# Performance work log

Hardware: AMD Instinct MI355X
Metric: run time of the kernel (lower is better)

Reference implementation:

```python
import jax, jax.numpy as jnp
import numpy as np

B, H, N, C, E, D, L_OUT, LAYERS = 16, 64, 512, 3, 128, 32, 12, 2


def setup_inputs() -> dict:
    key = jax.random.key(0)
    ks = jax.random.split(key, 16)
    nrm = lambda k, s, sc=1.0: jax.random.normal(k, s, jnp.float32) * sc
    adj = jax.random.uniform(ks[0], (N, N), jnp.float32)
    adj = adj / adj.sum(axis=-1, keepdims=True)  # row-normalized prior adjacency
    return {
        "x_input": nrm(ks[1], (B, H, N, C)),
        "adj": adj,
        "Wf": nrm(ks[2], (3, E, 3 * C), 0.1),
        "Uf": nrm(ks[3], (3, E, E), 0.05),
        "bf": jnp.zeros((3, E), jnp.float32),
        "E1f": nrm(ks[4], (N, D)),
        "E2f": nrm(ks[5], (N, D)),
        "Wb": nrm(ks[6], (3, E, 3 * C), 0.1),
        "Ub": nrm(ks[7], (3, E, E), 0.05),
        "bb": jnp.zeros((3, E), jnp.float32),
        "E1b": nrm(ks[8], (N, D)),
        "E2b": nrm(ks[9], (N, D)),
        "dec_w": nrm(ks[10], (L_OUT, LAYERS, 2 * E), 0.05),  # Conv2d(layer_num->out_len, k=(1,2E)) squeezed
        "dec_b": jnp.zeros((L_OUT,), jnp.float32),
        "out_w": nrm(ks[11], (L_OUT, L_OUT), 0.1),  # 1x1 Conv2d squeezed
        "out_b": jnp.zeros((L_OUT,), jnp.float32),
    }


def _cell_step(c, xt, adj, A_dyn, W, U, b):
    # Graph-coupled GRU cell (IBNCell): xt [B,C,N], c [B,E,N].
    msg = jnp.concatenate(
        [xt,
         jnp.einsum('bcn,nm->bcm', xt, adj),      # prior-graph message passing
         jnp.einsum('bcn,nm->bcm', xt, A_dyn)],   # learned dynamic-graph message passing
        axis=1)  # [B, 3C, N]
    gx = jnp.einsum('goc,bcn->gbon', W, msg)  # 3 stacked gate projections
    r = jax.nn.sigmoid(gx[0] + jnp.einsum('oe,ben->bon', U[0], c) + b[0][:, None])
    u = jax.nn.sigmoid(gx[1] + jnp.einsum('oe,ben->bon', U[1], c) + b[1][:, None])
    g = jnp.tanh(gx[2] + jnp.einsum('oe,ben->bon', U[2], r * c) + b[2][:, None])
    return u * c + (1.0 - u) * g


def _forward(x_input, adj, Wf, Uf, bf, E1f, E2f, Wb, Ub, bb, E1b, E2b, dec_w, dec_b, out_w, out_b):
    # torch: x_input.transpose(-3,-1).transpose(-2,-1) -> [B,C,H,N]; scan layout [H,B,C,N]
    xs = jnp.transpose(x_input, (1, 0, 3, 2))
    A_f = jax.nn.softmax(jax.nn.relu(E1f @ E2f.T), axis=-1)  # dynamic adjacency, fwd cell
    A_b = jax.nn.softmax(jax.nn.relu(E1b @ E2b.T), axis=-1)  # dynamic adjacency, back cell
    c0 = jnp.zeros((xs.shape[1], Wf.shape[1], xs.shape[3]), xs.dtype)  # [B,E,N]

    def step_f(c, xt):
        cn = _cell_step(c, xt, adj, A_f, Wf, Uf, bf)
        return cn, None

    # Output only depends on the last timestep of the bidirectional concat:
    # forward branch -> final state after H steps; backward branch (after flip)
    # at t=H-1 -> its FIRST step (input x[H-1]). Dead per-step outputs elided.
    h_fwd, _ = jax.lax.scan(step_f, c0, xs)
    h_back0 = _cell_step(c0, xs[-1], adj, A_b, Wb, Ub, bb)
    last_ht = jnp.concatenate([h_fwd, h_back0], axis=1)  # [B, 2E, N]

    lt = jnp.transpose(last_ht, (0, 2, 1))  # [B, N, 2E]
    # layer loop z>0 is a no-op on current_layer_output -> final_result repeats last_ht
    final = jnp.broadcast_to(lt[:, None], (lt.shape[0], LAYERS, lt.shape[1], lt.shape[2]))
    h = jnp.einsum('blne,ole->bon', final, dec_w) + dec_b[:, None]  # decoder conv (1,2E)
    return jnp.einsum('oi,bin->bon', out_w, h) + out_b[:, None]  # 1x1 output conv -> [B,L_OUT,N]


def reference(x_input, adj, Wf, Uf, bf, E1f, E2f, Wb, Ub, bb, E1b, E2b, dec_w, dec_b, out_w, out_b):
    return _forward(x_input, adj, Wf, Uf, bf, E1f, E2f, Wb, Ub, bb, E1b, E2b, dec_w, dec_b, out_w, out_b)
```

## Files before the change

### kernel.cpp

```cpp
#include <hip/hip_runtime.h>


typedef _Float16 half8_t __attribute__((ext_vector_type(8)));
typedef __fp16 fp16x2_t __attribute__((ext_vector_type(2)));
typedef float float4_t __attribute__((ext_vector_type(4)));

#define PIN(x) asm volatile("" : "+v"(x))

__device__ __forceinline__ float exp2_(float x) { return __builtin_amdgcn_exp2f(x); }
__device__ __forceinline__ float rcp_(float x) { return __builtin_amdgcn_rcpf(x); }

__global__ __launch_bounds__(256) void prep_kernel(
    const float* __restrict__ E1f, const float* __restrict__ E2f,
    const float* __restrict__ E1b, const float* __restrict__ E2b,
    const float* __restrict__ adj, const float* __restrict__ Wf,
    const float* __restrict__ Uf, const float* __restrict__ bf,
    const float* __restrict__ Wb, const float* __restrict__ bb,
    _Float16* __restrict__ adjT, _Float16* __restrict__ AfT,
    _Float16* __restrict__ AbT, _Float16* __restrict__ ufrag,
    _Float16* __restrict__ wbfrag, _Float16* __restrict__ zpad) {
  int bid = blockIdx.x;
  int tid = threadIdx.x;
  if (bid >= 1288) {
    if (tid < 64) zpad[tid] = (_Float16)0.f;
    return;
  }
  if (bid >= 1272) {
    int r2 = bid - 1272;
    int gi = 1 + (r2 & 1);
    int og = r2 >> 1;
    float scl = (gi == 2) ? 2.8853902f : -1.4426950f;
    for (int e = tid; e < 512; e += 256) {
      int lane = e >> 3, j = e & 7;
      int o = og * 16 + (lane & 15);
      int q = (lane >> 4) * 8 + j;
      float v = (q < 9) ? Wb[gi * 1152 + o * 9 + q]
                        : (q == 9 ? bb[gi * 128 + o] : 0.f);
      wbfrag[r2 * 512 + e] = (_Float16)(v * scl);
    }
    return;
  }
  if (bid >= 1152) {
    int r = bid - 1152;
    int kb = r % 5;
    int gi = (r / 5) % 3;
    int og = r / 15;
    float scl = (gi == 2) ? 2.8853902f : -1.4426950f;
    for (int e = tid; e < 512; e += 256) {
      int lane = e >> 3, j = e & 7;
      int o = og * 16 + (lane & 15);
      int q4 = lane >> 4;
      float v;
      if (kb < 4) {
        v = Uf[gi * 16384 + o * 128 + kb * 32 + q4 * 8 + j];
      } else {
        int q = q4 * 8 + j;
        v = (q < 9) ? Wf[gi * 1152 + o * 9 + q]
                    : (q == 9 ? bf[gi * 128 + o] : 0.f);
      }
      ufrag[r * 512 + e] = (_Float16)(v * scl);
    }
    return;
  }
  if (bid >= 1024) {
    int base = (bid - 1024) * 4;
    for (int r = 0; r < 4; ++r) {
      int row = base + r;
      float v0 = adj[row * 512 + tid];
      float v1 = adj[row * 512 + tid + 256];
      adjT[(size_t)tid * 512 + row] = (_Float16)v0;
      adjT[(size_t)(tid + 256) * 512 + row] = (_Float16)v1;
    }
    return;
  }
  int which = bid >> 9;
  int row = bid & 511;
  const float* E1 = which ? E1b : E1f;
  const float* E2 = which ? E2b : E2f;
  _Float16* A = which ? AbT : AfT;
  __shared__ float e1s[32];
  __shared__ float red[256];
  if (tid < 32) e1s[tid] = E1[row * 32 + tid];
  __syncthreads();
  float s[2];
#pragma unroll
  for (int h = 0; h < 2; ++h) {
    int m = tid + h * 256;
    const float4* e2 = (const float4*)(E2 + m * 32);
    float acc = 0.f;
#pragma unroll
    for (int d4 = 0; d4 < 8; ++d4) {
      float4 v = e2[d4];
      acc = fmaf(v.x, e1s[d4 * 4 + 0], acc);
      acc = fmaf(v.y, e1s[d4 * 4 + 1], acc);
      acc = fmaf(v.z, e1s[d4 * 4 + 2], acc);
      acc = fmaf(v.w, e1s[d4 * 4 + 3], acc);
    }
    s[h] = fmaxf(acc, 0.f);
  }
  red[tid] = fmaxf(s[0], s[1]);
  __syncthreads();
  for (int off = 128; off > 0; off >>= 1) {
    if (tid < off) red[tid] = fmaxf(red[tid], red[tid + off]);
    __syncthreads();
  }
  float mx = red[0];
  __syncthreads();
  float e0 = __expf(s[0] - mx), e1v = __expf(s[1] - mx);
  red[tid] = e0 + e1v;
  __syncthreads();
  for (int off = 128; off > 0; off >>= 1) {
    if (tid < off) red[tid] += red[tid + off];
    __syncthreads();
  }
  float inv = rcp_(red[0]);
  A[(size_t)tid * 512 + row] = (_Float16)(e0 * inv);
  A[(size_t)(tid + 256) * 512 + row] = (_Float16)(e1v * inv);
}

__global__ __launch_bounds__(256, 2) void msg_kernel(
    const float* __restrict__ x, const _Float16* __restrict__ adjT,
    const _Float16* __restrict__ AfT, const _Float16* __restrict__ AbT,
    _Float16* __restrict__ msg16, _Float16* __restrict__ msgb16) {
  __shared__ __align__(16) _Float16 Alds[48 * 512];
  __shared__ __align__(16) _Float16 Sst[1024 * 16];
  int tid = threadIdx.x;
  int t = blockIdx.x >> 3;
  int n0g = (blockIdx.x & 7) * 64;
  int lane = tid & 63, og = tid >> 6;
  int l15 = lane & 15, q4 = lane >> 4, q0 = q4 * 8;
  bool is63 = (t == 63);

  {
    int b = tid >> 4, li = tid & 15;
    const float4* xb = (const float4*)(x + (size_t)(b * 64 + t) * 1536);
#pragma unroll
    for (int k = 0; k < 24; ++k) {
      float4 v = xb[k * 16 + li];
      int j0 = (k * 16 + li) * 4;
#pragma unroll
      for (int e = 0; e < 4; ++e) {
        int j = j0 + e;
        int n = (j * 21846) >> 16;
        int c = j - n * 3;
        int m = b * 3 + c;
        float val = (e == 0) ? v.x : (e == 1) ? v.y : (e == 2) ? v.z : v.w;
        Alds[m * 512 + ((((n >> 3) ^ (m & 7)) << 3) | (n & 7))] = (_Float16)val;
      }
    }
  }
  __syncthreads();

  const float4_t zero4 = {0.f, 0.f, 0.f, 0.f};
  float4_t acc[3][2], accb[3];
#pragma unroll
  for (int mt = 0; mt < 3; ++mt) { acc[mt][0] = zero4; acc[mt][1] = zero4; accb[mt] = zero4; }

  int n = n0g + og * 16 + l15;
  for (int kb = 0; kb < 16; ++kb) {
    half8_t afr[3];
#pragma unroll
    for (int mt = 0; mt < 3; ++mt) {
      int m = mt * 16 + l15;
      afr[mt] = *(const half8_t*)&Alds[m * 512 + ((((kb * 4 + q4) ^ (m & 7)) << 3))];
    }
    half8_t b0 = *(const half8_t*)&adjT[(size_t)n * 512 + kb * 32 + q0];
    half8_t b1 = *(const half8_t*)&AfT[(size_t)n * 512 + kb * 32 + q0];
#pragma unroll
    for (int mt = 0; mt < 3; ++mt) {
      acc[mt][0] = __builtin_amdgcn_mfma_f32_16x16x32_f16(afr[mt], b0, acc[mt][0], 0, 0, 0);
      acc[mt][1] = __builtin_amdgcn_mfma_f32_16x16x32_f16(afr[mt], b1, acc[mt][1], 0, 0, 0);
    }
    if (is63) {
      half8_t b2 = *(const half8_t*)&AbT[(size_t)n * 512 + kb * 32 + q0];
#pragma unroll
      for (int mt = 0; mt < 3; ++mt)
        accb[mt] = __builtin_amdgcn_mfma_f32_16x16x32_f16(afr[mt], b2, accb[mt], 0, 0, 0);
    }
  }

  for (int i = tid; i < 1024; i += 256) {
    int tb = i >> 6, nl = i & 63;
    int nn = n0g + nl;
    _Float16* row = &Sst[i * 16];
#pragma unroll
    for (int c = 0; c < 3; ++c) {
      int m = tb * 3 + c;
      row[c] = Alds[m * 512 + ((((nn >> 3) ^ (m & 7)) << 3) | (nn & 7))];
    }
    row[9] = (_Float16)1.f;
#pragma unroll
    for (int z = 10; z < 16; ++z) row[z] = (_Float16)0.f;
  }
#pragma unroll
  for (int mt = 0; mt < 3; ++mt)
#pragma unroll
    for (int r = 0; r < 4; ++r) {
      int m = mt * 16 + q4 * 4 + r;
      int tb = (m * 21846) >> 16;
      int c = m - tb * 3;
      _Float16* row = &Sst[(tb * 64 + og * 16 + l15) * 16];
      row[3 + c] = (_Float16)acc[mt][0][r];
      row[6 + c] = (_Float16)acc[mt][1][r];
    }
  __syncthreads();
  for (int i = tid; i < 2048; i += 256) {
    int rrow = i >> 1, h = i & 1;
    int tb = rrow >> 6, nl = rrow & 63;
    ((uint4*)msg16)[(((size_t)(t * 16 + tb) * 512) + n0g + nl) * 2 + h] =
        ((const uint4*)Sst)[i];
  }
  if (is63) {
    __syncthreads();
#pragma unroll
    for (int mt = 0; mt < 3; ++mt)
#pragma unroll
      for (int r = 0; r < 4; ++r) {
        int m = mt * 16 + q4 * 4 + r;
        int tb = (m * 21846) >> 16;
        int c = m - tb * 3;
        Sst[(tb * 64 + og * 16 + l15) * 16 + 6 + c] = (_Float16)accb[mt][r];
      }
    __syncthreads();
    for (int i = tid; i < 2048; i += 256) {
      int rrow = i >> 1, h = i & 1;
      int tb = rrow >> 6, nl = rrow & 63;
      ((uint4*)msgb16)[(((size_t)tb * 512) + n0g + nl) * 2 + h] =
          ((const uint4*)Sst)[i];
    }
  }
}

__global__ __launch_bounds__(512, 4) void rec_kernel(
    const _Float16* __restrict__ msg16, const _Float16* __restrict__ msgb16,
    const _Float16* __restrict__ zpad, const _Float16* __restrict__ ufrag,
    const _Float16* __restrict__ wbfrag, const float* __restrict__ dec_w,
    const float* __restrict__ dec_b, const float* __restrict__ out_w,
    const float* __restrict__ out_b, float* __restrict__ out) {
  __shared__ __align__(16) _Float16 Cbuf[2048];
  __shared__ __align__(16) _Float16 Gbuf[2048];
  __shared__ float hf_lds[128 * 16];
  __shared__ float hb_lds[128 * 16];
  __shared__ float hdec_lds[12 * 16];
  int tid = threadIdx.x, bid = blockIdx.x;
  int b = bid >> 5;
  int nt = bid & 31;
  int n0 = nt * 16;
  int lane = tid & 63, og = tid >> 6;
  int l15 = lane & 15, q4 = lane >> 4;

  half8_t afrag[3][5];
#pragma unroll
  for (int gi = 0; gi < 3; ++gi)
#pragma unroll
    for (int kb = 0; kb < 5; ++kb) {
      afrag[gi][kb] = *(const half8_t*)
          &ufrag[(size_t)(((og * 3 + gi) * 5 + kb) * 512) + lane * 8];
      PIN(afrag[gi][kb]);
    }

  if (tid < 256) {
    uint4 z; z.x = z.y = z.z = z.w = 0;
    ((uint4*)Cbuf)[tid] = z;
  }
  float cr[4] = {0.f, 0.f, 0.f, 0.f};

  const float4_t zero4 = {0.f, 0.f, 0.f, 0.f};
  union H4U { fp16x2_t h2[2]; unsigned long long u; };
  const char* base = (const char*)msg16 +
                     ((size_t)(b * 512 + n0 + l15)) * 32 + (q4 & 1) * 16;
  const char* mrow = (q4 < 2) ? base : (const char*)zpad;
  size_t tstr = (q4 < 2) ? (size_t)16 * 512 * 32 : 0;
  half8_t bm = *(const half8_t*)mrow;

  int kb_w = og >> 1;
  int lane_w = ((og & 1) * 2 + (q4 >> 1)) * 16 + l15;
  int j0 = (q4 & 1) * 4;
  __syncthreads();

  for (int t = 0; t < 64; ++t) {
    int tn = (t < 63) ? t + 1 : 63;
    half8_t bm_n = *(const half8_t*)(mrow + (size_t)tn * tstr);

    half8_t cf[4];
#pragma unroll
    for (int kb = 0; kb < 4; ++kb)
      cf[kb] = *(const half8_t*)&Cbuf[(kb * 64 + lane) * 8];

    float4_t accr = zero4, accu = zero4;
#pragma unroll
    for (int kb = 0; kb < 4; ++kb) {
      accr = __builtin_amdgcn_mfma_f32_16x16x32_f16(afrag[0][kb], cf[kb], accr, 0, 0, 0);
      accu = __builtin_amdgcn_mfma_f32_16x16x32_f16(afrag[1][kb], cf[kb], accu, 0, 0, 0);
    }
    accr = __builtin_amdgcn_mfma_f32_16x16x32_f16(afrag[0][4], bm, accr, 0, 0, 0);
    accu = __builtin_amdgcn_mfma_f32_16x16x32_f16(afrag[1][4], bm, accu, 0, 0, 0);
    float4_t accg_p = __builtin_amdgcn_mfma_f32_16x16x32_f16(afrag[2][4], bm, zero4, 0, 0, 0);

    float uu[4];
    {
      H4U v;
#pragma unroll
      for (int r = 0; r < 2; ++r) {
        float a = rcp_(1.f + exp2_(accr[2 * r])) * cr[2 * r];
        float bq = rcp_(1.f + exp2_(accr[2 * r + 1])) * cr[2 * r + 1];
        v.h2[r] = __builtin_amdgcn_cvt_pkrtz(a, bq);
      }
      *(unsigned long long*)&Gbuf[(kb_w * 64 + lane_w) * 8 + j0] = v.u;
#pragma unroll
      for (int r = 0; r < 4; ++r) uu[r] = rcp_(1.f + exp2_(accu[r]));
    }
    __syncthreads();

    half8_t gf[4];
#pragma unroll
    for (int kb = 0; kb < 4; ++kb)
      gf[kb] = *(const half8_t*)&Gbuf[(kb * 64 + lane) * 8];
    float4_t accg = accg_p;
#pragma unroll
    for (int kb = 0; kb < 4; ++kb)
      accg = __builtin_amdgcn_mfma_f32_16x16x32_f16(afrag[2][kb], gf[kb], accg, 0, 0, 0);

    {
      H4U v;
      float cn[4];
#pragma unroll
      for (int r = 0; r < 4; ++r) {
        float gg = fmaf(-2.f, rcp_(exp2_(accg[r]) + 1.f), 1.f);
        cn[r] = fmaf(uu[r], cr[r] - gg, gg);
        cr[r] = cn[r];
      }
      v.h2[0] = __builtin_amdgcn_cvt_pkrtz(cn[0], cn[1]);
      v.h2[1] = __builtin_amdgcn_cvt_pkrtz(cn[2], cn[3]);
      *(unsigned long long*)&Cbuf[(kb_w * 64 + lane_w) * 8 + j0] = v.u;
    }
    __syncthreads();
    bm = bm_n;
  }

  {
    const char* bb_base = (const char*)msgb16 +
                          ((size_t)(b * 512 + n0 + l15)) * 32 + (q4 & 1) * 16;
    const char* bp = (q4 < 2) ? bb_base : (const char*)zpad;
    half8_t bbk = *(const half8_t*)bp;
    half8_t au_f = *(const half8_t*)&wbfrag[(size_t)((og * 2 + 0) * 512) + lane * 8];
    half8_t ag_f = *(const half8_t*)&wbfrag[(size_t)((og * 2 + 1) * 512) + lane * 8];
    float4_t au = __builtin_amdgcn_mfma_f32_16x16x32_f16(au_f, bbk, zero4, 0, 0, 0);
    float4_t ag = __builtin_amdgcn_mfma_f32_16x16x32_f16(ag_f, bbk, zero4, 0, 0, 0);
#pragma unroll
    for (int r = 0; r < 4; ++r) {
      int row = og * 16 + q4 * 4 + r;
      float uu2 = rcp_(1.f + exp2_(au[r]));
      float gg = fmaf(-2.f, rcp_(exp2_(ag[r]) + 1.f), 1.f);
      hb_lds[row * 16 + l15] = (1.f - uu2) * gg;
      hf_lds[row * 16 + l15] = cr[r];
    }
  }
  __syncthreads();

  if (tid < 192) {
    int i = tid >> 4, cc = tid & 15;
    const float* dwa = dec_w + (size_t)i * 512;
    const float* dwb = dwa + 256;
    float hd = dec_b[i];
    for (int e = 0; e < 128; ++e) {
      hd = fmaf(dwa[e] + dwb[e], hf_lds[e * 16 + cc], hd);
      hd = fmaf(dwa[128 + e] + dwb[128 + e], hb_lds[e * 16 + cc], hd);
    }
    hdec_lds[i * 16 + cc] = hd;
  }
  __syncthreads();
  if (tid < 192) {
    int o = tid >> 4, cc = tid & 15;
    float v = out_b[o];
#pragma unroll
    for (int i = 0; i < 12; ++i) v = fmaf(out_w[o * 12 + i], hdec_lds[i * 16 + cc], v);
    out[((size_t)(b * 12 + o)) * 512 + n0 + cc] = v;
  }
}

extern "C" void kernel_launch(void* const* d_in, const int* in_sizes, int n_in,
                              void* d_out, int out_size, void* d_ws, size_t ws_size,
                              hipStream_t stream) {
  (void)in_sizes; (void)n_in; (void)out_size; (void)ws_size;
  const float* x     = (const float*)d_in[0];
  const float* adj   = (const float*)d_in[1];
  const float* Wf    = (const float*)d_in[2];
  const float* Uf    = (const float*)d_in[3];
  const float* bf    = (const float*)d_in[4];
  const float* E1f   = (const float*)d_in[5];
  const float* E2f   = (const float*)d_in[6];
  const float* Wb    = (const float*)d_in[7];
  const float* bb    = (const float*)d_in[9];
  const float* E1b   = (const float*)d_in[10];
  const float* E2b   = (const float*)d_in[11];
  const float* dec_w = (const float*)d_in[12];
  const float* dec_b = (const float*)d_in[13];
  const float* out_w = (const float*)d_in[14];
  const float* out_b = (const float*)d_in[15];

  _Float16* h      = (_Float16*)d_ws;
  _Float16* adjT   = h;
  _Float16* AfT    = h + 262144;
  _Float16* AbT    = h + 524288;
  _Float16* ufrag  = h + 786432;
  _Float16* wbfrag = h + 847872;
  _Float16* zpad   = h + 856064;
  _Float16* msg16  = h + 856128;
  _Float16* msgb16 = h + 9244736;

  prep_kernel<<<1289, 256, 0, stream>>>(E1f, E2f, E1b, E2b, adj, Wf, Uf, bf,
                                        Wb, bb, adjT, AfT, AbT, ufrag, wbfrag, zpad);
  msg_kernel<<<512, 256, 0, stream>>>(x, adjT, AfT, AbT, msg16, msgb16);
  rec_kernel<<<512, 512, 0, stream>>>(msg16, msgb16, zpad, ufrag, wbfrag,
                                      dec_w, dec_b, out_w, out_b, (float*)d_out);
}
```

Baseline: 200.5 us.

## Fuse prep, message and recurrence kernels into one cooperative kernel with grid syncs

Merges the three launches into a single cooperative kernel of 512 blocks of 512 threads, separated by grid-wide barriers, with a fallback to three launches if the cooperative launch fails. The message phase is reshaped so that each wave computes one matrix (adj, A_f, A_b) over two 32-column halves, and the prep phase is remapped to 512-thread blocks. The goal is to remove launch gaps and tail effects between kernels. In exchange it adds grid-sync cost, occupancy limits from the 64KB shared buffer and 512-thread blocks, and a less efficient msg phase in which AbT work is done by every block.

```diff
diff --git a/kernel.cpp b/kernel.cpp
--- a/kernel.cpp
+++ b/kernel.cpp
@@ -1,4 +1,7 @@
 #include <hip/hip_runtime.h>
+#include <hip/hip_cooperative_groups.h>
+
+namespace cg = cooperative_groups;
 
 
 typedef _Float16 half8_t __attribute__((ext_vector_type(8)));
@@ -10,83 +13,26 @@
 __device__ __forceinline__ float exp2_(float x) { return __builtin_amdgcn_exp2f(x); }
 __device__ __forceinline__ float rcp_(float x) { return __builtin_amdgcn_rcpf(x); }
 
-__global__ __launch_bounds__(256) void prep_kernel(
-    const float* __restrict__ E1f, const float* __restrict__ E2f,
-    const float* __restrict__ E1b, const float* __restrict__ E2b,
-    const float* __restrict__ adj, const float* __restrict__ Wf,
-    const float* __restrict__ Uf, const float* __restrict__ bf,
-    const float* __restrict__ Wb, const float* __restrict__ bb,
-    _Float16* __restrict__ adjT, _Float16* __restrict__ AfT,
-    _Float16* __restrict__ AbT, _Float16* __restrict__ ufrag,
-    _Float16* __restrict__ wbfrag, _Float16* __restrict__ zpad) {
-  int bid = blockIdx.x;
-  int tid = threadIdx.x;
-  if (bid >= 1288) {
-    if (tid < 64) zpad[tid] = (_Float16)0.f;
-    return;
-  }
-  if (bid >= 1272) {
-    int r2 = bid - 1272;
-    int gi = 1 + (r2 & 1);
-    int og = r2 >> 1;
-    float scl = (gi == 2) ? 2.8853902f : -1.4426950f;
-    for (int e = tid; e < 512; e += 256) {
-      int lane = e >> 3, j = e & 7;
-      int o = og * 16 + (lane & 15);
-      int q = (lane >> 4) * 8 + j;
-      float v = (q < 9) ? Wb[gi * 1152 + o * 9 + q]
-                        : (q == 9 ? bb[gi * 128 + o] : 0.f);
-      wbfrag[r2 * 512 + e] = (_Float16)(v * scl);
-    }
-    return;
-  }
-  if (bid >= 1152) {
-    int r = bid - 1152;
-    int kb = r % 5;
-    int gi = (r / 5) % 3;
-    int og = r / 15;
-    float scl = (gi == 2) ? 2.8853902f : -1.4426950f;
-    for (int e = tid; e < 512; e += 256) {
-      int lane = e >> 3, j = e & 7;
-      int o = og * 16 + (lane & 15);
-      int q4 = lane >> 4;
-      float v;
-      if (kb < 4) {
-        v = Uf[gi * 16384 + o * 128 + kb * 32 + q4 * 8 + j];
-      } else {
-        int q = q4 * 8 + j;
-        v = (q < 9) ? Wf[gi * 1152 + o * 9 + q]
-                    : (q == 9 ? bf[gi * 128 + o] : 0.f);
-      }
-      ufrag[r * 512 + e] = (_Float16)(v * scl);
-    }
-    return;
-  }
-  if (bid >= 1024) {
-    int base = (bid - 1024) * 4;
-    for (int r = 0; r < 4; ++r) {
-      int row = base + r;
-      float v0 = adj[row * 512 + tid];
-      float v1 = adj[row * 512 + tid + 256];
-      adjT[(size_t)tid * 512 + row] = (_Float16)v0;
-      adjT[(size_t)(tid + 256) * 512 + row] = (_Float16)v1;
-    }
-    return;
-  }
-  int which = bid >> 9;
-  int row = bid & 511;
-  const float* E1 = which ? E1b : E1f;
-  const float* E2 = which ? E2b : E2f;
-  _Float16* A = which ? AbT : AfT;
-  __shared__ float e1s[32];
-  __shared__ float red[256];
-  if (tid < 32) e1s[tid] = E1[row * 32 + tid];
-  __syncthreads();
-  float s[2];
-#pragma unroll
-  for (int h = 0; h < 2; ++h) {
-    int m = tid + h * 256;
-    const float4* e2 = (const float4*)(E2 + m * 32);
+struct P {
+  const float *E1f, *E2f, *E1b, *E2b, *adj, *x, *Wf, *Uf, *bf, *Wb, *bb;
+  const float *dec_w, *dec_b, *out_w, *out_b;
+  float* out;
+  _Float16 *adjT, *AfT, *AbT, *ufrag, *wbfrag, *zpad, *msg16, *msgb16;
+};
+
+__device__ void phase_prep(const P& p, char* smem, int bid, int tid) {
+  float* red = (float*)smem;
+  float* e1s = (float*)(smem + 2048);
+  for (int rr = 0; rr < 2; ++rr) {
+    int rowid = bid * 2 + rr;
+    int which = rowid >> 9, row = rowid & 511;
+    const float* E1 = which ? p.E1b : p.E1f;
+    const float* E2 = which ? p.E2b : p.E2f;
+    _Float16* A = which ? p.AbT : p.AfT;
+    __syncthreads();
+    if (tid < 32) e1s[tid] = E1[row * 32 + tid];
+    __syncthreads();
+    const float4* e2 = (const float4*)(E2 + tid * 32);
     float acc = 0.f;
 #pragma unroll
     for (int d4 = 0; d4 < 8; ++d4) {
@@ -96,48 +42,77 @@
       acc = fmaf(v.z, e1s[d4 * 4 + 2], acc);
       acc = fmaf(v.w, e1s[d4 * 4 + 3], acc);
     }
-    s[h] = fmaxf(acc, 0.f);
-  }
-  red[tid] = fmaxf(s[0], s[1]);
-  __syncthreads();
-  for (int off = 128; off > 0; off >>= 1) {
-    if (tid < off) red[tid] = fmaxf(red[tid], red[tid + off]);
-    __syncthreads();
-  }
-  float mx = red[0];
-  __syncthreads();
-  float e0 = __expf(s[0] - mx), e1v = __expf(s[1] - mx);
-  red[tid] = e0 + e1v;
-  __syncthreads();
-  for (int off = 128; off > 0; off >>= 1) {
-    if (tid < off) red[tid] += red[tid + off];
-    __syncthreads();
-  }
-  float inv = rcp_(red[0]);
-  A[(size_t)tid * 512 + row] = (_Float16)(e0 * inv);
-  A[(size_t)(tid + 256) * 512 + row] = (_Float16)(e1v * inv);
-}
-
-__global__ __launch_bounds__(256, 2) void msg_kernel(
-    const float* __restrict__ x, const _Float16* __restrict__ adjT,
-    const _Float16* __restrict__ AfT, const _Float16* __restrict__ AbT,
-    _Float16* __restrict__ msg16, _Float16* __restrict__ msgb16) {
-  __shared__ __align__(16) _Float16 Alds[48 * 512];
-  __shared__ __align__(16) _Float16 Sst[1024 * 16];
-  int tid = threadIdx.x;
-  int t = blockIdx.x >> 3;
-  int n0g = (blockIdx.x & 7) * 64;
+    float s = fmaxf(acc, 0.f);
+    red[tid] = s;
+    __syncthreads();
+    for (int off = 256; off > 0; off >>= 1) {
+      if (tid < off) red[tid] = fmaxf(red[tid], red[tid + off]);
+      __syncthreads();
+    }
+    float mx = red[0];
+    __syncthreads();
+    float e0 = __expf(s - mx);
+    red[tid] = e0;
+    __syncthreads();
+    for (int off = 256; off > 0; off >>= 1) {
+      if (tid < off) red[tid] += red[tid + off];
+      __syncthreads();
+    }
+    float inv = rcp_(red[0]);
+    A[(size_t)tid * 512 + row] = (_Float16)(e0 * inv);
+  }
+  if (bid < 128) {
+    int base = bid * 4;
+    for (int r = 0; r < 4; ++r) {
+      int row = base + r;
+      p.adjT[(size_t)tid * 512 + row] = (_Float16)p.adj[row * 512 + tid];
+    }
+  } else if (bid < 248) {
+    int r = bid - 128;
+    int kb = r % 5, gi = (r / 5) % 3, og = r / 15;
+    float scl = (gi == 2) ? 2.8853902f : -1.4426950f;
+    int lane = tid >> 3, j = tid & 7;
+    int o = og * 16 + (lane & 15);
+    int q4 = lane >> 4;
+    float v;
+    if (kb < 4) {
+      v = p.Uf[gi * 16384 + o * 128 + kb * 32 + q4 * 8 + j];
+    } else {
+      int q = q4 * 8 + j;
+      v = (q < 9) ? p.Wf[gi * 1152 + o * 9 + q]
+                  : (q == 9 ? p.bf[gi * 128 + o] : 0.f);
+    }
+    p.ufrag[r * 512 + tid] = (_Float16)(v * scl);
+  } else if (bid < 264) {
+    int r2 = bid - 248;
+    int gi = 1 + (r2 & 1), og = r2 >> 1;
+    float scl = (gi == 2) ? 2.8853902f : -1.4426950f;
+    int lane = tid >> 3, j = tid & 7;
+    int o = og * 16 + (lane & 15);
+    int q = (lane >> 4) * 8 + j;
+    float v = (q < 9) ? p.Wb[gi * 1152 + o * 9 + q]
+                      : (q == 9 ? p.bb[gi * 128 + o] : 0.f);
+    p.wbfrag[r2 * 512 + tid] = (_Float16)(v * scl);
+  } else if (bid == 264) {
+    if (tid < 64) p.zpad[tid] = (_Float16)0.f;
+  }
+}
+
+__device__ void phase_msg(const P& p, char* smem, int bid, int tid) {
+  _Float16* Alds = (_Float16*)smem;
+  _Float16* Sst = (_Float16*)(smem + 49152);
+  int t = bid >> 3;
+  bool is63 = (t == 63);
   int lane = tid & 63, og = tid >> 6;
   int l15 = lane & 15, q4 = lane >> 4, q0 = q4 * 8;
-  bool is63 = (t == 63);
 
   {
-    int b = tid >> 4, li = tid & 15;
-    const float4* xb = (const float4*)(x + (size_t)(b * 64 + t) * 1536);
-#pragma unroll
-    for (int k = 0; k < 24; ++k) {
-      float4 v = xb[k * 16 + li];
-      int j0 = (k * 16 + li) * 4;
+    int b = tid >> 5, li = tid & 31;
+    const float4* xb = (const float4*)(p.x + (size_t)(b * 64 + t) * 1536);
+#pragma unroll
+    for (int k = 0; k < 12; ++k) {
+      float4 v = xb[k * 32 + li];
+      int j0 = (k * 32 + li) * 4;
 #pragma unroll
       for (int e = 0; e < 4; ++e) {
         int j = j0 + e;
@@ -151,98 +126,91 @@
   }
   __syncthreads();
 
+  int nt = og & 1, mat = og >> 1;
   const float4_t zero4 = {0.f, 0.f, 0.f, 0.f};
-  float4_t acc[3][2], accb[3];
-#pragma unroll
-  for (int mt = 0; mt < 3; ++mt) { acc[mt][0] = zero4; acc[mt][1] = zero4; accb[mt] = zero4; }
-
-  int n = n0g + og * 16 + l15;
-  for (int kb = 0; kb < 16; ++kb) {
-    half8_t afr[3];
-#pragma unroll
-    for (int mt = 0; mt < 3; ++mt) {
-      int m = mt * 16 + l15;
-      afr[mt] = *(const half8_t*)&Alds[m * 512 + ((((kb * 4 + q4) ^ (m & 7)) << 3))];
-    }
-    half8_t b0 = *(const half8_t*)&adjT[(size_t)n * 512 + kb * 32 + q0];
-    half8_t b1 = *(const half8_t*)&AfT[(size_t)n * 512 + kb * 32 + q0];
-#pragma unroll
-    for (int mt = 0; mt < 3; ++mt) {
-      acc[mt][0] = __builtin_amdgcn_mfma_f32_16x16x32_f16(afr[mt], b0, acc[mt][0], 0, 0, 0);
-      acc[mt][1] = __builtin_amdgcn_mfma_f32_16x16x32_f16(afr[mt], b1, acc[mt][1], 0, 0, 0);
+  for (int half = 0; half < 2; ++half) {
+    int nc = (bid & 7) + half * 8;
+    int n0g = nc * 32;
+    float4_t acc[3];
+    acc[0] = zero4; acc[1] = zero4; acc[2] = zero4;
+    if (og < 6) {
+      const _Float16* Bmat = (mat == 0) ? p.adjT : (mat == 1) ? p.AfT : p.AbT;
+      int n = n0g + nt * 16 + l15;
+      for (int kb = 0; kb < 16; ++kb) {
+        half8_t b0 = *(const half8_t*)&Bmat[(size_t)n * 512 + kb * 32 + q0];
+#pragma unroll
+        for (int mt = 0; mt < 3; ++mt) {
+          int m = mt * 16 + l15;
+          half8_t a = *(const half8_t*)
+              &Alds[m * 512 + ((((kb * 4 + q4) ^ (m & 7)) << 3))];
+          acc[mt] = __builtin_amdgcn_mfma_f32_16x16x32_f16(a, b0, acc[mt], 0, 0, 0);
+        }
+      }
+    } else {
+      int lt = (og - 6) * 64 + lane;
+      for (int i = lt; i < 512; i += 128) {
+        int tb = i >> 5, nl = i & 31;
+        int nn = n0g + nl;
+        _Float16* row = &Sst[i * 16];
+#pragma unroll
+        for (int c = 0; c < 3; ++c) {
+          int m = tb * 3 + c;
+          row[c] = Alds[m * 512 + ((((nn >> 3) ^ (m & 7)) << 3) | (nn & 7))];
+        }
+        row[9] = (_Float16)1.f;
+#pragma unroll
+        for (int z = 10; z < 16; ++z) row[z] = (_Float16)0.f;
+      }
+    }
+    if (og < 6 && mat < 2) {
+#pragma unroll
+      for (int mt = 0; mt < 3; ++mt)
+#pragma unroll
+        for (int r = 0; r < 4; ++r) {
+          int m = mt * 16 + q4 * 4 + r;
+          int tb = (m * 21846) >> 16;
+          int c = m - tb * 3;
+          Sst[(tb * 32 + nt * 16 + l15) * 16 + 3 + mat * 3 + c] = (_Float16)acc[mt][r];
+        }
+    }
+    __syncthreads();
+    for (int i = tid; i < 1024; i += 512) {
+      int rrow = i >> 1, h = i & 1;
+      int tb = rrow >> 5, nl = rrow & 31;
+      ((uint4*)p.msg16)[(((size_t)(t * 16 + tb) * 512) + n0g + nl) * 2 + h] =
+          ((const uint4*)Sst)[i];
     }
     if (is63) {
-      half8_t b2 = *(const half8_t*)&AbT[(size_t)n * 512 + kb * 32 + q0];
-#pragma unroll
-      for (int mt = 0; mt < 3; ++mt)
-        accb[mt] = __builtin_amdgcn_mfma_f32_16x16x32_f16(afr[mt], b2, accb[mt], 0, 0, 0);
-    }
-  }
-
-  for (int i = tid; i < 1024; i += 256) {
-    int tb = i >> 6, nl = i & 63;
-    int nn = n0g + nl;
-    _Float16* row = &Sst[i * 16];
-#pragma unroll
-    for (int c = 0; c < 3; ++c) {
-      int m = tb * 3 + c;
-      row[c] = Alds[m * 512 + ((((nn >> 3) ^ (m & 7)) << 3) | (nn & 7))];
-    }
-    row[9] = (_Float16)1.f;
-#pragma unroll
-    for (int z = 10; z < 16; ++z) row[z] = (_Float16)0.f;
-  }
-#pragma unroll
-  for (int mt = 0; mt < 3; ++mt)
-#pragma unroll
-    for (int r = 0; r < 4; ++r) {
-      int m = mt * 16 + q4 * 4 + r;
-      int tb = (m * 21846) >> 16;
-      int c = m - tb * 3;
-      _Float16* row = &Sst[(tb * 64 + og * 16 + l15) * 16];
-      row[3 + c] = (_Float16)acc[mt][0][r];
-      row[6 + c] = (_Float16)acc[mt][1][r];
-    }
-  __syncthreads();
-  for (int i = tid; i < 2048; i += 256) {
-    int rrow = i >> 1, h = i & 1;
-    int tb = rrow >> 6, nl = rrow & 63;
-    ((uint4*)msg16)[(((size_t)(t * 16 + tb) * 512) + n0g + nl) * 2 + h] =
-        ((const uint4*)Sst)[i];
-  }
-  if (is63) {
-    __syncthreads();
-#pragma unroll
-    for (int mt = 0; mt < 3; ++mt)
-#pragma unroll
-      for (int r = 0; r < 4; ++r) {
-        int m = mt * 16 + q4 * 4 + r;
-        int tb = (m * 21846) >> 16;
-        int c = m - tb * 3;
-        Sst[(tb * 64 + og * 16 + l15) * 16 + 6 + c] = (_Float16)accb[mt][r];
-      }
-    __syncthreads();
-    for (int i = tid; i < 2048; i += 256) {
-      int rrow = i >> 1, h = i & 1;
-      int tb = rrow >> 6, nl = rrow & 63;
-      ((uint4*)msgb16)[(((size_t)tb * 512) + n0g + nl) * 2 + h] =
-          ((const uint4*)Sst)[i];
-    }
-  }
-}
-
-__global__ __launch_bounds__(512, 4) void rec_kernel(
-    const _Float16* __restrict__ msg16, const _Float16* __restrict__ msgb16,
-    const _Float16* __restrict__ zpad, const _Float16* __restrict__ ufrag,
-    const _Float16* __restrict__ wbfrag, const float* __restrict__ dec_w,
-    const float* __restrict__ dec_b, const float* __restrict__ out_w,
-    const float* __restrict__ out_b, float* __restrict__ out) {
-  __shared__ __align__(16) _Float16 Cbuf[2048];
-  __shared__ __align__(16) _Float16 Gbuf[2048];
-  __shared__ float hf_lds[128 * 16];
-  __shared__ float hb_lds[128 * 16];
-  __shared__ float hdec_lds[12 * 16];
-  int tid = threadIdx.x, bid = blockIdx.x;
+      __syncthreads();
+      if (og < 6 && mat == 2) {
+#pragma unroll
+        for (int mt = 0; mt < 3; ++mt)
+#pragma unroll
+          for (int r = 0; r < 4; ++r) {
+            int m = mt * 16 + q4 * 4 + r;
+            int tb = (m * 21846) >> 16;
+            int c = m - tb * 3;
+            Sst[(tb * 32 + nt * 16 + l15) * 16 + 6 + c] = (_Float16)acc[mt][r];
+          }
+      }
+      __syncthreads();
+      for (int i = tid; i < 1024; i += 512) {
+        int rrow = i >> 1, h = i & 1;
+        int tb = rrow >> 5, nl = rrow & 31;
+        ((uint4*)p.msgb16)[(((size_t)tb * 512) + n0g + nl) * 2 + h] =
+            ((const uint4*)Sst)[i];
+      }
+    }
+    __syncthreads();
+  }
+}
+
+__device__ void phase_rec(const P& p, char* smem, int bid, int tid) {
+  _Float16* Cbuf = (_Float16*)smem;
+  _Float16* Gbuf = (_Float16*)(smem + 4096);
+  float* hf_lds = (float*)(smem + 8192);
+  float* hb_lds = (float*)(smem + 16384);
+  float* hdec_lds = (float*)(smem + 24576);
   int b = bid >> 5;
   int nt = bid & 31;
   int n0 = nt * 16;
@@ -255,7 +223,7 @@
 #pragma unroll
     for (int kb = 0; kb < 5; ++kb) {
       afrag[gi][kb] = *(const half8_t*)
-          &ufrag[(size_t)(((og * 3 + gi) * 5 + kb) * 512) + lane * 8];
+          &p.ufrag[(size_t)(((og * 3 + gi) * 5 + kb) * 512) + lane * 8];
       PIN(afrag[gi][kb]);
     }
 
@@ -267,9 +235,9 @@
 
   const float4_t zero4 = {0.f, 0.f, 0.f, 0.f};
   union H4U { fp16x2_t h2[2]; unsigned long long u; };
-  const char* base = (const char*)msg16 +
+  const char* base = (const char*)p.msg16 +
                      ((size_t)(b * 512 + n0 + l15)) * 32 + (q4 & 1) * 16;
-  const char* mrow = (q4 < 2) ? base : (const char*)zpad;
+  const char* mrow = (q4 < 2) ? base : (const char*)p.zpad;
   size_t tstr = (q4 < 2) ? (size_t)16 * 512 * 32 : 0;
   half8_t bm = *(const half8_t*)mrow;
 
@@ -339,12 +307,12 @@
   }
 
   {
-    const char* bb_base = (const char*)msgb16 +
+    const char* bb_base = (const char*)p.msgb16 +
                           ((size_t)(b * 512 + n0 + l15)) * 32 + (q4 & 1) * 16;
-    const char* bp = (q4 < 2) ? bb_base : (const char*)zpad;
+    const char* bp = (q4 < 2) ? bb_base : (const char*)p.zpad;
     half8_t bbk = *(const half8_t*)bp;
-    half8_t au_f = *(const half8_t*)&wbfrag[(size_t)((og * 2 + 0) * 512) + lane * 8];
-    half8_t ag_f = *(const half8_t*)&wbfrag[(size_t)((og * 2 + 1) * 512) + lane * 8];
+    half8_t au_f = *(const half8_t*)&p.wbfrag[(size_t)((og * 2 + 0) * 512) + lane * 8];
+    half8_t ag_f = *(const half8_t*)&p.wbfrag[(size_t)((og * 2 + 1) * 512) + lane * 8];
     float4_t au = __builtin_amdgcn_mfma_f32_16x16x32_f16(au_f, bbk, zero4, 0, 0, 0);
     float4_t ag = __builtin_amdgcn_mfma_f32_16x16x32_f16(ag_f, bbk, zero4, 0, 0, 0);
 #pragma unroll
@@ -360,9 +328,9 @@
 
   if (tid < 192) {
     int i = tid >> 4, cc = tid & 15;
-    const float* dwa = dec_w + (size_t)i * 512;
+    const float* dwa = p.dec_w + (size_t)i * 512;
     const float* dwb = dwa + 256;
-    float hd = dec_b[i];
+    float hd = p.dec_b[i];
     for (int e = 0; e < 128; ++e) {
       hd = fmaf(dwa[e] + dwb[e], hf_lds[e * 16 + cc], hd);
       hd = fmaf(dwa[128 + e] + dwb[128 + e], hb_lds[e * 16 + cc], hd);
@@ -372,46 +340,75 @@
   __syncthreads();
   if (tid < 192) {
     int o = tid >> 4, cc = tid & 15;
-    float v = out_b[o];
-#pragma unroll
-    for (int i = 0; i < 12; ++i) v = fmaf(out_w[o * 12 + i], hdec_lds[i * 16 + cc], v);
-    out[((size_t)(b * 12 + o)) * 512 + n0 + cc] = v;
-  }
+    float v = p.out_b[o];
+#pragma unroll
+    for (int i = 0; i < 12; ++i)
+      v = fmaf(p.out_w[o * 12 + i], hdec_lds[i * 16 + cc], v);
+    p.out[((size_t)(b * 12 + o)) * 512 + n0 + cc] = v;
+  }
+}
+
+__global__ __launch_bounds__(512, 4) void fused_kernel(P p) {
+  __shared__ __align__(16) char smem[65536];
+  cg::grid_group grid = cg::this_grid();
+  phase_prep(p, smem, blockIdx.x, threadIdx.x);
+  grid.sync();
+  phase_msg(p, smem, blockIdx.x, threadIdx.x);
+  grid.sync();
+  phase_rec(p, smem, blockIdx.x, threadIdx.x);
+}
+
+__global__ __launch_bounds__(512, 4) void prep_k(P p) {
+  __shared__ __align__(16) char smem[65536];
+  phase_prep(p, smem, blockIdx.x, threadIdx.x);
+}
+__global__ __launch_bounds__(512, 4) void msg_k(P p) {
+  __shared__ __align__(16) char smem[65536];
+  phase_msg(p, smem, blockIdx.x, threadIdx.x);
+}
+__global__ __launch_bounds__(512, 4) void rec_k(P p) {
+  __shared__ __align__(16) char smem[65536];
+  phase_rec(p, smem, blockIdx.x, threadIdx.x);
 }
 
 extern "C" void kernel_launch(void* const* d_in, const int* in_sizes, int n_in,
                               void* d_out, int out_size, void* d_ws, size_t ws_size,
                               hipStream_t stream) {
   (void)in_sizes; (void)n_in; (void)out_size; (void)ws_size;
-  const float* x     = (const float*)d_in[0];
-  const float* adj   = (const float*)d_in[1];
-  const float* Wf    = (const float*)d_in[2];
-  const float* Uf    = (const float*)d_in[3];
-  const float* bf    = (const float*)d_in[4];
-  const float* E1f   = (const float*)d_in[5];
-  const float* E2f   = (const float*)d_in[6];
-  const float* Wb    = (const float*)d_in[7];
-  const float* bb    = (const float*)d_in[9];
-  const float* E1b   = (const float*)d_in[10];
-  const float* E2b   = (const float*)d_in[11];
-  const float* dec_w = (const float*)d_in[12];
-  const float* dec_b = (const float*)d_in[13];
-  const float* out_w = (const float*)d_in[14];
-  const float* out_b = (const float*)d_in[15];
-
-  _Float16* h      = (_Float16*)d_ws;
-  _Float16* adjT   = h;
-  _Float16* AfT    = h + 262144;
-  _Float16* AbT    = h + 524288;
-  _Float16* ufrag  = h + 786432;
-  _Float16* wbfrag = h + 847872;
-  _Float16* zpad   = h + 856064;
-  _Float16* msg16  = h + 856128;
-  _Float16* msgb16 = h + 9244736;
-
-  prep_kernel<<<1289, 256, 0, stream>>>(E1f, E2f, E1b, E2b, adj, Wf, Uf, bf,
-                                        Wb, bb, adjT, AfT, AbT, ufrag, wbfrag, zpad);
-  msg_kernel<<<512, 256, 0, stream>>>(x, adjT, AfT, AbT, msg16, msgb16);
-  rec_kernel<<<512, 512, 0, stream>>>(msg16, msgb16, zpad, ufrag, wbfrag,
-                                      dec_w, dec_b, out_w, out_b, (float*)d_out);
-}
+  _Float16* h = (_Float16*)d_ws;
+  P p;
+  p.E1f = (const float*)d_in[5];
+  p.E2f = (const float*)d_in[6];
+  p.E1b = (const float*)d_in[10];
+  p.E2b = (const float*)d_in[11];
+  p.adj = (const float*)d_in[1];
+  p.x   = (const float*)d_in[0];
+  p.Wf  = (const float*)d_in[2];
+  p.Uf  = (const float*)d_in[3];
+  p.bf  = (const float*)d_in[4];
+  p.Wb  = (const float*)d_in[7];
+  p.bb  = (const float*)d_in[9];
+  p.dec_w = (const float*)d_in[12];
+  p.dec_b = (const float*)d_in[13];
+  p.out_w = (const float*)d_in[14];
+  p.out_b = (const float*)d_in[15];
+  p.out = (float*)d_out;
+  p.adjT   = h;
+  p.AfT    = h + 262144;
+  p.AbT    = h + 524288;
+  p.ufrag  = h + 786432;
+  p.wbfrag = h + 847872;
+  p.zpad   = h + 856064;
+  p.msg16  = h + 856128;
+  p.msgb16 = h + 9244736;
+
+  void* args[] = {&p};
+  hipError_t err = hipLaunchCooperativeKernel((const void*)fused_kernel,
+                                              dim3(512), dim3(512), args, 0, stream);
+  if (err != hipSuccess) {
+    (void)hipGetLastError();
+    prep_k<<<512, 512, 0, stream>>>(p);
+    msg_k<<<512, 512, 0, stream>>>(p);
+    rec_k<<<512, 512, 0, stream>>>(p);
+  }
+}
```

New measurement: 356.5 us. 77.8% more time.
